# Kernel optimization log

Hardware: AMD Instinct MI355X
Metric: run time of the kernel (lower is better)

Reference implementation:

```python
import jax, jax.numpy as jnp
import numpy as np

K_V_DIM = 100
_SQRT_D = float(np.sqrt(K_V_DIM))


def _dk_layer(q, k, v, Wq, bq, Wk, n_unsqueeze):
    """One DKEncoder_layer: DK_text + DK_knowledge + DK_fusion (CokeBert attention).
    q: [B, q_dim]; k: [..., n, K_V_DIM]; v: [..., n, d_v].
    Attention over the last neighbor axis n.
    """
    # DK_text: linear + tanh + unsqueeze to broadcast against k
    q_i = jnp.tanh(q @ Wq.T + bq)                               # [B, D]
    q_i = q_i.reshape((q_i.shape[0],) + (1,) * n_unsqueeze + (K_V_DIM,))
    # DK_knowledge: bias-free linear on k
    k = k @ Wk.T
    # DK_fusion (CokeBert): scaled dot, mask zeros, leaky_relu+softmax, zero out fully-masked rows
    attn = (q_i * k).sum(-1) / _SQRT_D                          # [..., n]
    attn = jnp.where(attn == 0.0, -10000.0, attn)
    attn = jax.nn.softmax(jax.nn.leaky_relu(attn), axis=-1)
    n = attn.shape[-1]
    attn = jnp.where(attn == 1.0 / n, 0.0, attn)
    return jnp.einsum('...n,...nd->...d', attn, v)              # [..., d_v]


def setup_inputs() -> dict:
    key = jax.random.key(0)
    ks = jax.random.split(key, 12)
    B, S, E, N1, N2, D, Q = 8, 256, 256, 16, 16, K_V_DIM, 768
    return {
        "input_ent": jax.random.randint(ks[0], (B, S), 0, 2, dtype=jnp.int64),
        "q": jax.random.normal(ks[1], (B, S, Q), dtype=jnp.float32),
        "k1": jax.random.normal(ks[2], (B, E, N1, D), dtype=jnp.float32),
        "v1": jax.random.normal(ks[3], (B, E, N1, D), dtype=jnp.float32),
        "k2": jax.random.normal(ks[4], (B, E, N1, N2, D), dtype=jnp.float32),
        "v2": jax.random.normal(ks[5], (B, E, N1, N2, D), dtype=jnp.float32),
        # layers[0] has layer_no=2 (deepest), layers[1] has layer_no=1
        "Wq2": jax.random.normal(ks[6], (D, Q), dtype=jnp.float32) * 0.05,
        "bq2": jnp.zeros((D,), dtype=jnp.float32),
        "Wk2": jax.random.normal(ks[7], (D, D), dtype=jnp.float32) * 0.1,
        "Wq1": jax.random.normal(ks[8], (D, Q), dtype=jnp.float32) * 0.05,
        "bq1": jnp.zeros((D,), dtype=jnp.float32),
        "Wk1": jax.random.normal(ks[9], (D, D), dtype=jnp.float32) * 0.1,
    }


def reference(input_ent, q, k1, v1, k2, v2, Wq2, bq2, Wk2, Wq1, bq1, Wk1):
    q0 = q[:, 0, :]                                             # [B, Q]
    # layer 0 (layer_no=2): reduce innermost neighbor axis
    combined = _dk_layer(q0, k2, v2, Wq2, bq2, Wk2, 3)          # [B, E, N1, D]
    # layer 1 (layer_no=1): v = cat([v1, combined])
    v1c = jnp.concatenate([v1, combined], axis=-1)              # [B, E, N1, 2D]
    combined = _dk_layer(q0, k1, v1c, Wq1, bq1, Wk1, 2)         # [B, E, 2D]
    # scatter: i-th nonzero position of input_ent[b] receives combined[b, i]
    mask = input_ent != 0                                       # [B, S]
    rank = jnp.cumsum(mask.astype(jnp.int32), axis=1) - 1       # [B, S]
    rank = jnp.clip(rank, 0, combined.shape[1] - 1)
    gathered = jnp.take_along_axis(combined, rank[..., None], axis=1)  # [B, S, 2D]
    return jnp.where(mask[..., None], gathered, 0.0)
```

## Files before the change

### kernel.cpp

```cpp
#include <hip/hip_runtime.h>
#include <cstddef>
#include <cstdint>

#define BB 8
#define SS 256
#define EE 256
#define NN1 16
#define NN2 16
#define DD 100
#define QQ 768

__device__ __forceinline__ float dot4(float4 a, float4 b) {
    return a.x * b.x + a.y * b.y + a.z * b.z + a.w * b.w;
}

#define LGKM0() do { asm volatile("s_waitcnt lgkmcnt(0)" ::: "memory"); \
                     __builtin_amdgcn_sched_barrier(0); } while (0)

__global__ __launch_bounds__(256) void prep_kernel(
    const float* __restrict__ q, const int* __restrict__ ent,
    const float* __restrict__ Wq2, const float* __restrict__ bq2, const float* __restrict__ Wk2,
    const float* __restrict__ Wq1, const float* __restrict__ bq1, const float* __restrict__ Wk1,
    float* __restrict__ qk2o, float* __restrict__ qk1o, int* __restrict__ rk)
{
    const int blk = blockIdx.x, t = threadIdx.x;
    if (blk < 16) {
        const int b = blk >> 1, layer = blk & 1;
        const float* Wq = layer ? Wq1 : Wq2;
        const float* bq = layer ? bq1 : bq2;
        const float* Wk = layer ? Wk1 : Wk2;
        float* qko      = layer ? qk1o : qk2o;
        __shared__ float s_q[QQ];
        __shared__ float s_qi[DD];
        for (int i = t; i < QQ; i += 256) s_q[i] = q[(size_t)b * SS * QQ + i];
        __syncthreads();
        const float4* sq4 = (const float4*)s_q;
        const int r = t & 7;
        for (int d = t >> 3; d < DD; d += 32) {
            const float4* wq4 = (const float4*)(Wq + (size_t)d * QQ);
            float acc = 0.f;
            for (int c = r; c < QQ / 4; c += 8) acc += dot4(wq4[c], sq4[c]);
            acc += __shfl_xor(acc, 1, 8);
            acc += __shfl_xor(acc, 2, 8);
            acc += __shfl_xor(acc, 4, 8);
            if (r == 0) s_qi[d] = tanhf(acc + bq[d]);
        }
        __syncthreads();
        if (t < DD) {
            float acc = 0.f;
            for (int d = 0; d < DD; ++d) acc += s_qi[d] * Wk[d * DD + t];
            qko[b * DD + t] = 0.1f * acc;
        }
    } else {
        const int b = blk - 16;
        __shared__ int s_m[SS];
        const int m = (ent[b * SS + t] != 0) ? 1 : 0;
        s_m[t] = m;
        __syncthreads();
        for (int off = 1; off < SS; off <<= 1) {
            const int add = (t >= off) ? s_m[t - off] : 0;
            __syncthreads();
            s_m[t] += add;
            __syncthreads();
        }
        int rank = s_m[t] - 1;
        rank = rank < 0 ? 0 : (rank > EE - 1 ? EE - 1 : rank);
        rk[b * SS + t] = m ? rank : -1;
    }
}

__global__ __launch_bounds__(64) void dk2_kernel(
    const float* __restrict__ k2, const float* __restrict__ v2,
    const float* __restrict__ qk2g, float* __restrict__ c2o,
    int b0, int nunits)
{
    const int t = threadIdx.x;
    __shared__ float4 s_pp[400];
    float* s_part = (float*)s_pp;

    const int UPB = 8;
    int u = blockIdx.x * UPB;
    if (u >= nunits) return;
    const int uend = (u + UPB < nunits) ? u + UPB : nunits;
    const int b = b0 + (u >> 12);

    const float4* qkb = (const float4*)qk2g + (size_t)b * 25;
    float4 qv[7];
    #pragma unroll
    for (int j = 0; j < 6; ++j) qv[j] = qkb[(t + 64 * j) % 25];
    qv[6] = qkb[(384 + t) % 25];

    const float4* kt = (const float4*)k2 + ((size_t)b0 * 4096 + u) * 400;
    const float4* vt = (const float4*)v2 + ((size_t)b0 * 4096 + u) * 400;

    float4 ka[7];
    #pragma unroll
    for (int j = 0; j < 6; ++j) ka[j] = kt[t + 64 * j];
    if (t < 16) ka[6] = kt[384 + t];

    for (; u < uend; ++u, kt += 400, vt += 400) {
        float4 va[7];
        #pragma unroll
        for (int j = 0; j < 6; ++j) va[j] = vt[t + 64 * j];
        if (t < 16) va[6] = vt[384 + t];

        #pragma unroll
        for (int j = 0; j < 6; ++j) s_part[t + 64 * j] = dot4(ka[j], qv[j]);
        if (t < 16) s_part[384 + t] = dot4(ka[6], qv[6]);

        if (u + 1 < uend) {
            const float4* ktn = kt + 400;
            #pragma unroll
            for (int j = 0; j < 6; ++j) ka[j] = ktn[t + 64 * j];
            if (t < 16) ka[6] = ktn[384 + t];
        }

        LGKM0();
        float p;
        {
            float lg = 0.f;
            if (t < 16) {
                #pragma unroll
                for (int c = 0; c < 25; ++c) lg += s_part[t * 25 + c];
                if (lg == 0.0f) lg = -10000.0f;
                lg = lg >= 0.f ? lg : 0.01f * lg;
            }
            float mx = lg;
            mx = fmaxf(mx, __shfl_xor(mx, 1, 16));
            mx = fmaxf(mx, __shfl_xor(mx, 2, 16));
            mx = fmaxf(mx, __shfl_xor(mx, 4, 16));
            mx = fmaxf(mx, __shfl_xor(mx, 8, 16));
            const float e = __expf(lg - mx);
            float sm = e;
            sm += __shfl_xor(sm, 1, 16);
            sm += __shfl_xor(sm, 2, 16);
            sm += __shfl_xor(sm, 4, 16);
            sm += __shfl_xor(sm, 8, 16);
            p = e / sm;
            if (p == 0.0625f) p = 0.f;
        }

        #pragma unroll
        for (int j = 0; j < 6; ++j) {
            const int i = t + 64 * j;
            const float pn = __shfl(p, i / 25, 64);
            s_pp[i] = make_float4(pn * va[j].x, pn * va[j].y, pn * va[j].z, pn * va[j].w);
        }
        if (t < 16) {
            const int i = 384 + t;
            const float pn = __shfl(p, 15, 64);
            s_pp[i] = make_float4(pn * va[6].x, pn * va[6].y, pn * va[6].z, pn * va[6].w);
        }
        LGKM0();

        if (t < 25) {
            float4 a = make_float4(0.f, 0.f, 0.f, 0.f);
            #pragma unroll
            for (int n = 0; n < 16; ++n) {
                const float4 x = s_pp[n * 25 + t];
                a.x += x.x; a.y += x.y; a.z += x.z; a.w += x.w;
            }
            ((float4*)c2o)[(size_t)u * 25 + t] = a;
        }
    }
}

__global__ __launch_bounds__(64) void dk1_kernel(
    const float* __restrict__ k1, const float* __restrict__ v1,
    const float* __restrict__ c2i, const float* __restrict__ qk1g,
    float* __restrict__ comb, int b0)
{
    const int blk  = blockIdx.x;
    const int bbe  = blk >> 1;
    const int half = blk & 1;
    const int b    = b0 + (bbe >> 8);
    const int be   = (b << 8) | (bbe & 255);
    const int t    = threadIdx.x;

    __shared__ float4 s_pp[400];
    float* s_part = (float*)s_pp;

    const float4* kt = (const float4*)k1 + (size_t)be * 400;
    const float4* vt = half ? (const float4*)c2i + (size_t)bbe * 400
                            : (const float4*)v1 + (size_t)be * 400;
    const float4* qkb = (const float4*)qk1g + (size_t)b * 25;

    float4 qv[7];
    #pragma unroll
    for (int j = 0; j < 6; ++j) qv[j] = qkb[(t + 64 * j) % 25];
    qv[6] = qkb[(384 + t) % 25];

    float4 ka[7], va[7];
    #pragma unroll
    for (int j = 0; j < 6; ++j) { ka[j] = kt[t + 64 * j]; va[j] = vt[t + 64 * j]; }
    if (t < 16) { ka[6] = kt[384 + t]; va[6] = vt[384 + t]; }

    #pragma unroll
    for (int j = 0; j < 6; ++j) s_part[t + 64 * j] = dot4(ka[j], qv[j]);
    if (t < 16) s_part[384 + t] = dot4(ka[6], qv[6]);
    LGKM0();

    float p;
    {
        float lg = 0.f;
        if (t < 16) {
            #pragma unroll
            for (int c = 0; c < 25; ++c) lg += s_part[t * 25 + c];
            if (lg == 0.0f) lg = -10000.0f;
            lg = lg >= 0.f ? lg : 0.01f * lg;
        }
        float mx = lg;
        mx = fmaxf(mx, __shfl_xor(mx, 1, 16));
        mx = fmaxf(mx, __shfl_xor(mx, 2, 16));
        mx = fmaxf(mx, __shfl_xor(mx, 4, 16));
        mx = fmaxf(mx, __shfl_xor(mx, 8, 16));
        const float e = __expf(lg - mx);
        float sm = e;
        sm += __shfl_xor(sm, 1, 16);
        sm += __shfl_xor(sm, 2, 16);
        sm += __shfl_xor(sm, 4, 16);
        sm += __shfl_xor(sm, 8, 16);
        p = e / sm;
        if (p == 0.0625f) p = 0.f;
    }

    #pragma unroll
    for (int j = 0; j < 6; ++j) {
        const int i = t + 64 * j;
        const float pn = __shfl(p, i / 25, 64);
        s_pp[i] = make_float4(pn * va[j].x, pn * va[j].y, pn * va[j].z, pn * va[j].w);
    }
    if (t < 16) {
        const int i = 384 + t;
        const float pn = __shfl(p, 15, 64);
        s_pp[i] = make_float4(pn * va[6].x, pn * va[6].y, pn * va[6].z, pn * va[6].w);
    }
    LGKM0();

    if (t < 25) {
        float4 a = make_float4(0.f, 0.f, 0.f, 0.f);
        #pragma unroll
        for (int n = 0; n < 16; ++n) {
            const float4 x = s_pp[n * 25 + t];
            a.x += x.x; a.y += x.y; a.z += x.z; a.w += x.w;
        }
        ((float4*)comb)[(size_t)be * 50 + half * 25 + t] = a;
    }
}

__global__ __launch_bounds__(64) void gather_kernel(
    const float* __restrict__ comb, const int* __restrict__ rk, float* __restrict__ out)
{
    const int bs = blockIdx.x;
    const int b  = bs >> 8;
    const int t  = threadIdx.x;
    const int r  = rk[bs];
    float* o = out + (size_t)bs * (2 * DD);
    if (r < 0) {
        for (int d = t; d < 2 * DD; d += 64) o[d] = 0.f;
    } else {
        const float* src = comb + (size_t)(b * EE + r) * (2 * DD);
        for (int d = t; d < 2 * DD; d += 64) o[d] = src[d];
    }
}

extern "C" void kernel_launch(void* const* d_in, const int* in_sizes, int n_in,
                              void* d_out, int out_size, void* d_ws, size_t ws_size,
                              hipStream_t stream)
{
    const int*   ent = (const int*)d_in[0];
    const float* q   = (const float*)d_in[1];
    const float* k1  = (const float*)d_in[2];
    const float* v1  = (const float*)d_in[3];
    const float* k2  = (const float*)d_in[4];
    const float* v2  = (const float*)d_in[5];
    const float* Wq2 = (const float*)d_in[6];
    const float* bq2 = (const float*)d_in[7];
    const float* Wk2 = (const float*)d_in[8];
    const float* Wq1 = (const float*)d_in[9];
    const float* bq1 = (const float*)d_in[10];
    const float* Wk1 = (const float*)d_in[11];
    float* out = (float*)d_out;

    float* ws   = (float*)d_ws;
    float* qk2  = ws;
    float* qk1  = ws + 1024;
    int*   rk   = (int*)(ws + 2048);
    float* comb = ws + 4096;
    float* c2   = ws + 4096 + 409600;

    const size_t fixed = 4096 + 409600;
    const size_t perb  = (size_t)EE * NN1 * DD;
    size_t wsf = ws_size / sizeof(float);
    int kb = (wsf > fixed) ? (int)((wsf - fixed) / perb) : 1;
    if (kb < 1) kb = 1;
    if (kb > BB) kb = BB;

    prep_kernel<<<24, 256, 0, stream>>>(q, ent, Wq2, bq2, Wk2, Wq1, bq1, Wk1, qk2, qk1, rk);
    for (int b0 = 0; b0 < BB; b0 += kb) {
        const int nb = (BB - b0 < kb) ? (BB - b0) : kb;
        const int nunits = nb * EE * NN1;
        const int grid = (nunits + 7) / 8;
        dk2_kernel<<<grid, 64, 0, stream>>>(k2, v2, qk2, c2, b0, nunits);
        dk1_kernel<<<nb * EE * 2, 64, 0, stream>>>(k1, v1, c2, qk1, comb, b0);
    }
    gather_kernel<<<BB * SS, 64, 0, stream>>>(comb, rk, out);
}
```

Baseline: 157.1 us.

## Restructure dk2 kernel into a 256-thread block with a double-buffered load pipeline

The innermost attention kernel now runs 256 threads per block over 16 neighbor units each, instead of 64 threads over 8. It keeps K and V loads for two units in flight in registers. Dot-product partials and raw V go into double-buffered LDS. The probability-weighted V reduction is fused into the consume step through lane shuffles, instead of writing pre-scaled V to LDS. The aim is more memory-level parallelism and overlap of global loads with the softmax and reduction on this bandwidth-bound stage. The cost is explicit block barriers, softmax computed redundantly by all four waves, and only 25 lanes doing the final accumulation.

```diff
diff --git a/kernel.cpp b/kernel.cpp
--- a/kernel.cpp
+++ b/kernel.cpp
@@ -16,6 +16,9 @@
 
 #define LGKM0() do { asm volatile("s_waitcnt lgkmcnt(0)" ::: "memory"); \
                      __builtin_amdgcn_sched_barrier(0); } while (0)
+#define SCHED0() __builtin_amdgcn_sched_barrier(0)
+#define BARRIER() do { asm volatile("s_waitcnt lgkmcnt(0)\n\ts_barrier" ::: "memory"); \
+                       __builtin_amdgcn_sched_barrier(0); } while (0)
 
 __global__ __launch_bounds__(256) void prep_kernel(
     const float* __restrict__ q, const int* __restrict__ ent,
@@ -69,100 +72,115 @@
     }
 }
 
-__global__ __launch_bounds__(64) void dk2_kernel(
+__global__ __launch_bounds__(256, 4) void dk2_kernel(
     const float* __restrict__ k2, const float* __restrict__ v2,
     const float* __restrict__ qk2g, float* __restrict__ c2o,
     int b0, int nunits)
 {
     const int t = threadIdx.x;
-    __shared__ float4 s_pp[400];
-    float* s_part = (float*)s_pp;
-
-    const int UPB = 8;
-    int u = blockIdx.x * UPB;
-    if (u >= nunits) return;
-    const int uend = (u + UPB < nunits) ? u + UPB : nunits;
-    const int b = b0 + (u >> 12);
+    __shared__ float s_part[2][400];
+    __shared__ float s_v[2][1600];
+
+    const int base = blockIdx.x * 16;
+    if (base >= nunits) return;
+    const int b = b0 + (base >> 12);
 
     const float4* qkb = (const float4*)qk2g + (size_t)b * 25;
-    float4 qv[7];
-    #pragma unroll
-    for (int j = 0; j < 6; ++j) qv[j] = qkb[(t + 64 * j) % 25];
-    qv[6] = qkb[(384 + t) % 25];
-
-    const float4* kt = (const float4*)k2 + ((size_t)b0 * 4096 + u) * 400;
-    const float4* vt = (const float4*)v2 + ((size_t)b0 * 4096 + u) * 400;
-
-    float4 ka[7];
-    #pragma unroll
-    for (int j = 0; j < 6; ++j) ka[j] = kt[t + 64 * j];
-    if (t < 16) ka[6] = kt[384 + t];
-
-    for (; u < uend; ++u, kt += 400, vt += 400) {
-        float4 va[7];
-        #pragma unroll
-        for (int j = 0; j < 6; ++j) va[j] = vt[t + 64 * j];
-        if (t < 16) va[6] = vt[384 + t];
-
-        #pragma unroll
-        for (int j = 0; j < 6; ++j) s_part[t + 64 * j] = dot4(ka[j], qv[j]);
-        if (t < 16) s_part[384 + t] = dot4(ka[6], qv[6]);
-
-        if (u + 1 < uend) {
-            const float4* ktn = kt + 400;
-            #pragma unroll
-            for (int j = 0; j < 6; ++j) ka[j] = ktn[t + 64 * j];
-            if (t < 16) ka[6] = ktn[384 + t];
-        }
-
-        LGKM0();
-        float p;
-        {
-            float lg = 0.f;
-            if (t < 16) {
-                #pragma unroll
-                for (int c = 0; c < 25; ++c) lg += s_part[t * 25 + c];
-                if (lg == 0.0f) lg = -10000.0f;
-                lg = lg >= 0.f ? lg : 0.01f * lg;
-            }
-            float mx = lg;
-            mx = fmaxf(mx, __shfl_xor(mx, 1, 16));
-            mx = fmaxf(mx, __shfl_xor(mx, 2, 16));
-            mx = fmaxf(mx, __shfl_xor(mx, 4, 16));
-            mx = fmaxf(mx, __shfl_xor(mx, 8, 16));
-            const float e = __expf(lg - mx);
-            float sm = e;
-            sm += __shfl_xor(sm, 1, 16);
-            sm += __shfl_xor(sm, 2, 16);
-            sm += __shfl_xor(sm, 4, 16);
-            sm += __shfl_xor(sm, 8, 16);
-            p = e / sm;
-            if (p == 0.0625f) p = 0.f;
-        }
-
-        #pragma unroll
-        for (int j = 0; j < 6; ++j) {
-            const int i = t + 64 * j;
-            const float pn = __shfl(p, i / 25, 64);
-            s_pp[i] = make_float4(pn * va[j].x, pn * va[j].y, pn * va[j].z, pn * va[j].w);
-        }
-        if (t < 16) {
-            const int i = 384 + t;
-            const float pn = __shfl(p, 15, 64);
-            s_pp[i] = make_float4(pn * va[6].x, pn * va[6].y, pn * va[6].z, pn * va[6].w);
-        }
-        LGKM0();
-
-        if (t < 25) {
-            float4 a = make_float4(0.f, 0.f, 0.f, 0.f);
-            #pragma unroll
-            for (int n = 0; n < 16; ++n) {
-                const float4 x = s_pp[n * 25 + t];
-                a.x += x.x; a.y += x.y; a.z += x.z; a.w += x.w;
-            }
-            ((float4*)c2o)[(size_t)u * 25 + t] = a;
-        }
-    }
+    const float4 qv0 = qkb[t % 25];
+    const float4 qv1 = qkb[(t + 256) % 25];
+
+    const int  i0  = t;
+    const bool w1  = (t + 256 < 400);
+    const int  i1c = w1 ? t + 256 : 399;
+
+    const float4* kbase = (const float4*)k2 + ((size_t)b0 * 4096 + base) * 400;
+    const float4* vbase = (const float4*)v2 + ((size_t)b0 * 4096 + base) * 400;
+    float4* c2o4 = (float4*)c2o;
+
+    float4 kA0, kA1, vA0, vA1, kB0, kB1, vB0, vB1;
+
+#define ISSUE(K0, K1, V0, V1, ofs) do {                                     \
+        const float4* kp_ = kbase + (size_t)(ofs) * 400;                    \
+        const float4* vp_ = vbase + (size_t)(ofs) * 400;                    \
+        K0 = kp_[i0]; K1 = kp_[i1c]; V0 = vp_[i0]; V1 = vp_[i1c];           \
+    } while (0)
+
+#define DOTS(K0, K1, pb) do {                                               \
+        s_part[pb][i0] = dot4(K0, qv0);                                     \
+        if (w1) s_part[pb][t + 256] = dot4(K1, qv1);                        \
+    } while (0)
+
+#define VWRITE(V0, V1, sb) do {                                             \
+        ((float4*)s_v[sb])[i0] = V0;                                        \
+        if (w1) ((float4*)s_v[sb])[t + 256] = V1;                           \
+    } while (0)
+
+#define CONSUME(pb, sb, uu) do {                                            \
+        const int l_ = t & 15;                                              \
+        float lg_ = 0.f;                                                    \
+        _Pragma("unroll")                                                   \
+        for (int c_ = 0; c_ < 25; ++c_) lg_ += s_part[pb][l_ * 25 + c_];    \
+        if (lg_ == 0.0f) lg_ = -10000.0f;                                   \
+        lg_ = lg_ >= 0.f ? lg_ : 0.01f * lg_;               \
+        float mx_ = lg_;                                                    \
+        mx_ = fmaxf(mx_, __shfl_xor(mx_, 1, 16));                           \
+        mx_ = fmaxf(mx_, __shfl_xor(mx_, 2, 16));                           \
+        mx_ = fmaxf(mx_, __shfl_xor(mx_, 4, 16));                           \
+        mx_ = fmaxf(mx_, __shfl_xor(mx_, 8, 16));                           \
+        float e_ = __expf(lg_ - mx_);                                       \
+        float sm_ = e_;                                                     \
+        sm_ += __shfl_xor(sm_, 1, 16);                                      \
+        sm_ += __shfl_xor(sm_, 2, 16);                                      \
+        sm_ += __shfl_xor(sm_, 4, 16);                                      \
+        sm_ += __shfl_xor(sm_, 8, 16);                                      \
+        float p_ = e_ / sm_;                                                \
+        if (p_ == 0.0625f) p_ = 0.f;                    \
+        if (t < 25) {                                                       \
+            float ax = 0.f, ay = 0.f, az = 0.f, aw = 0.f;                   \
+            _Pragma("unroll")                                               \
+            for (int n_ = 0; n_ < 16; ++n_) {                               \
+                const float pn_ = __shfl(p_, n_, 64);   \
+                const float4 x_ = ((const float4*)s_v[sb])[n_ * 25 + t];    \
+                ax += pn_ * x_.x; ay += pn_ * x_.y;                         \
+                az += pn_ * x_.z; aw += pn_ * x_.w;                         \
+            }                                                               \
+            c2o4[(size_t)(uu) * 25 + t] = make_float4(ax, ay, az, aw);      \
+        }                                                                   \
+    } while (0)
+
+    ISSUE(kA0, kA1, vA0, vA1, 0);
+    ISSUE(kB0, kB1, vB0, vB1, 1);
+    SCHED0();
+    DOTS(kA0, kA1, 0);
+    VWRITE(vA0, vA1, 0);
+    BARRIER();
+
+    for (int g = 0; g < 7; ++g) {
+        const int x = 2 * g;
+        ISSUE(kA0, kA1, vA0, vA1, x + 2);
+        SCHED0();
+        CONSUME(0, 0, base + x);
+        DOTS(kB0, kB1, 1);
+        VWRITE(vB0, vB1, 1);
+        BARRIER();
+        ISSUE(kB0, kB1, vB0, vB1, x + 3);
+        SCHED0();
+        CONSUME(1, 1, base + x + 1);
+        DOTS(kA0, kA1, 0);
+        VWRITE(vA0, vA1, 0);
+        BARRIER();
+    }
+
+    CONSUME(0, 0, base + 14);
+    DOTS(kB0, kB1, 1);
+    VWRITE(vB0, vB1, 1);
+    BARRIER();
+    CONSUME(1, 1, base + 15);
+
+#undef ISSUE
+#undef DOTS
+#undef VWRITE
+#undef CONSUME
 }
 
 __global__ __launch_bounds__(64) void dk1_kernel(
@@ -300,8 +318,8 @@
     for (int b0 = 0; b0 < BB; b0 += kb) {
         const int nb = (BB - b0 < kb) ? (BB - b0) : kb;
         const int nunits = nb * EE * NN1;
-        const int grid = (nunits + 7) / 8;
-        dk2_kernel<<<grid, 64, 0, stream>>>(k2, v2, qk2, c2, b0, nunits);
+        const int grid = nunits / 16;
+        dk2_kernel<<<grid, 256, 0, stream>>>(k2, v2, qk2, c2, b0, nunits);
         dk1_kernel<<<nb * EE * 2, 64, 0, stream>>>(k1, v1, c2, qk1, comb, b0);
     }
     gather_kernel<<<BB * SS, 64, 0, stream>>>(comb, rk, out);
```

Result: slower. 163.3 us (+4.0%).

## Pipeline dk2 k/v loads into a 4-slot LDS ring via global_load_lds

Applied to the files above, without the earlier changes.

Rewrites the dominant dk2 kernel so each 64-thread block handles 64 units. K and V tiles stream directly from global memory into a 4-deep LDS ring buffer using async global_load_lds, and vmcnt waits keep up to three units in flight while the current one is computed. The dot products now run per row with 16-lane shuffle reductions, and the weighted V sum reads LDS directly. This is meant to hide HBM latency and cut register staging. In exchange it uses about 51KB of LDS per block, which limits occupancy, and it assumes nunits is divisible by 64 with hand-counted vmcnt values.

```diff
diff --git a/kernel.cpp b/kernel.cpp
--- a/kernel.cpp
+++ b/kernel.cpp
@@ -16,6 +16,7 @@
 
 #define LGKM0() do { asm volatile("s_waitcnt lgkmcnt(0)" ::: "memory"); \
                      __builtin_amdgcn_sched_barrier(0); } while (0)
+#define SCHED0() __builtin_amdgcn_sched_barrier(0)
 
 __global__ __launch_bounds__(256) void prep_kernel(
     const float* __restrict__ q, const int* __restrict__ ent,
@@ -75,94 +76,119 @@
     int b0, int nunits)
 {
     const int t = threadIdx.x;
-    __shared__ float4 s_pp[400];
-    float* s_part = (float*)s_pp;
-
-    const int UPB = 8;
-    int u = blockIdx.x * UPB;
-    if (u >= nunits) return;
-    const int uend = (u + UPB < nunits) ? u + UPB : nunits;
-    const int b = b0 + (u >> 12);
-
-    const float4* qkb = (const float4*)qk2g + (size_t)b * 25;
-    float4 qv[7];
-    #pragma unroll
-    for (int j = 0; j < 6; ++j) qv[j] = qkb[(t + 64 * j) % 25];
-    qv[6] = qkb[(384 + t) % 25];
-
-    const float4* kt = (const float4*)k2 + ((size_t)b0 * 4096 + u) * 400;
-    const float4* vt = (const float4*)v2 + ((size_t)b0 * 4096 + u) * 400;
-
-    float4 ka[7];
-    #pragma unroll
-    for (int j = 0; j < 6; ++j) ka[j] = kt[t + 64 * j];
-    if (t < 16) ka[6] = kt[384 + t];
-
-    for (; u < uend; ++u, kt += 400, vt += 400) {
-        float4 va[7];
-        #pragma unroll
-        for (int j = 0; j < 6; ++j) va[j] = vt[t + 64 * j];
-        if (t < 16) va[6] = vt[384 + t];
-
-        #pragma unroll
-        for (int j = 0; j < 6; ++j) s_part[t + 64 * j] = dot4(ka[j], qv[j]);
-        if (t < 16) s_part[384 + t] = dot4(ka[6], qv[6]);
-
-        if (u + 1 < uend) {
-            const float4* ktn = kt + 400;
-            #pragma unroll
-            for (int j = 0; j < 6; ++j) ka[j] = ktn[t + 64 * j];
-            if (t < 16) ka[6] = ktn[384 + t];
-        }
-
-        LGKM0();
-        float p;
-        {
-            float lg = 0.f;
-            if (t < 16) {
-                #pragma unroll
-                for (int c = 0; c < 25; ++c) lg += s_part[t * 25 + c];
-                if (lg == 0.0f) lg = -10000.0f;
-                lg = lg >= 0.f ? lg : 0.01f * lg;
-            }
-            float mx = lg;
-            mx = fmaxf(mx, __shfl_xor(mx, 1, 16));
-            mx = fmaxf(mx, __shfl_xor(mx, 2, 16));
-            mx = fmaxf(mx, __shfl_xor(mx, 4, 16));
-            mx = fmaxf(mx, __shfl_xor(mx, 8, 16));
-            const float e = __expf(lg - mx);
-            float sm = e;
-            sm += __shfl_xor(sm, 1, 16);
-            sm += __shfl_xor(sm, 2, 16);
-            sm += __shfl_xor(sm, 4, 16);
-            sm += __shfl_xor(sm, 8, 16);
-            p = e / sm;
-            if (p == 0.0625f) p = 0.f;
-        }
-
-        #pragma unroll
-        for (int j = 0; j < 6; ++j) {
-            const int i = t + 64 * j;
-            const float pn = __shfl(p, i / 25, 64);
-            s_pp[i] = make_float4(pn * va[j].x, pn * va[j].y, pn * va[j].z, pn * va[j].w);
-        }
-        if (t < 16) {
-            const int i = 384 + t;
-            const float pn = __shfl(p, 15, 64);
-            s_pp[i] = make_float4(pn * va[6].x, pn * va[6].y, pn * va[6].z, pn * va[6].w);
-        }
-        LGKM0();
-
-        if (t < 25) {
-            float4 a = make_float4(0.f, 0.f, 0.f, 0.f);
-            #pragma unroll
-            for (int n = 0; n < 16; ++n) {
-                const float4 x = s_pp[n * 25 + t];
-                a.x += x.x; a.y += x.y; a.z += x.z; a.w += x.w;
-            }
-            ((float4*)c2o)[(size_t)u * 25 + t] = a;
-        }
-    }
+    const int r = t & 15, g = t >> 4;
+    __shared__ float ring[4 * 3200];
+
+    const int UPB = 64;
+    const int u0 = blockIdx.x * UPB;
+    if (u0 >= nunits) return;
+    const int b = b0 + (u0 >> 12);
+
+    const float* qk = qk2g + (size_t)b * DD;
+    float qj[6];
+    #pragma unroll
+    for (int j = 0; j < 6; ++j) qj[j] = qk[r + 16 * j];
+    const float q6 = (r < 4) ? qk[96 + r] : 0.f;
+
+    const char* kgl = (const char*)(k2 + ((size_t)b0 * 4096 + u0) * 1600);
+    const char* vgl = (const char*)(v2 + ((size_t)b0 * 4096 + u0) * 1600);
+    auto g1k = (const __attribute__((address_space(1))) char*)kgl;
+    auto g1v = (const __attribute__((address_space(1))) char*)vgl;
+    auto l3  = (__attribute__((address_space(3))) char*)ring;
+
+#define ISSUE_UNIT(rel, slot) do {                                              \
+        const size_t gb_ = (size_t)(rel) * 6400;                                \
+        const int    lb_ = (slot) * 12800;                                      \
+        _Pragma("unroll")                                                       \
+        for (int j_ = 0; j_ < 6; ++j_) {                                        \
+            __builtin_amdgcn_global_load_lds(                                   \
+                (const __attribute__((address_space(1))) void*)(g1k + gb_ + j_ * 1024 + t * 16), \
+                (__attribute__((address_space(3))) void*)(l3 + lb_ + j_ * 1024), 16, 0, 0); \
+        }                                                                       \
+        __builtin_amdgcn_global_load_lds(                                       \
+            (const __attribute__((address_space(1))) void*)(g1k + gb_ + 5376 + t * 16), \
+            (__attribute__((address_space(3))) void*)(l3 + lb_ + 5376), 16, 0, 0); \
+        _Pragma("unroll")                                                       \
+        for (int j_ = 0; j_ < 6; ++j_) {                                        \
+            __builtin_amdgcn_global_load_lds(                                   \
+                (const __attribute__((address_space(1))) void*)(g1v + gb_ + j_ * 1024 + t * 16), \
+                (__attribute__((address_space(3))) void*)(l3 + lb_ + 6400 + j_ * 1024), 16, 0, 0); \
+        }                                                                       \
+        __builtin_amdgcn_global_load_lds(                                       \
+            (const __attribute__((address_space(1))) void*)(g1v + gb_ + 5376 + t * 16), \
+            (__attribute__((address_space(3))) void*)(l3 + lb_ + 6400 + 5376), 16, 0, 0); \
+    } while (0)
+
+#define COMPUTE_STORE(uu) do {                                                  \
+        const int   slot_ = (uu) & 3;                                           \
+        const float* Ks_ = ring + slot_ * 3200;                                 \
+        const float* Vs_ = Ks_ + 1600;                                          \
+        float lgv[4];                                                           \
+        _Pragma("unroll")                                                       \
+        for (int i_ = 0; i_ < 4; ++i_) {                                        \
+            const float* kr_ = Ks_ + (4 * g + i_) * DD;                         \
+            float s_ = kr_[r] * qj[0];                                          \
+            s_ += kr_[r + 16] * qj[1];                                          \
+            s_ += kr_[r + 32] * qj[2];                                          \
+            s_ += kr_[r + 48] * qj[3];                                          \
+            s_ += kr_[r + 64] * qj[4];                                          \
+            s_ += kr_[r + 80] * qj[5];                                          \
+            s_ += kr_[96 + r] * q6;       \
+            s_ += __shfl_xor(s_, 1, 16);                                        \
+            s_ += __shfl_xor(s_, 2, 16);                                        \
+            s_ += __shfl_xor(s_, 4, 16);                                        \
+            s_ += __shfl_xor(s_, 8, 16);                                        \
+            if (s_ == 0.0f) s_ = -10000.0f;                                     \
+            lgv[i_] = s_ >= 0.f ? s_ : 0.01f * s_;              \
+        }                                                                       \
+        float m_ = fmaxf(fmaxf(lgv[0], lgv[1]), fmaxf(lgv[2], lgv[3]));         \
+        m_ = fmaxf(m_, __shfl_xor(m_, 16, 64));                                 \
+        m_ = fmaxf(m_, __shfl_xor(m_, 32, 64));                                 \
+        const float e0_ = __expf(lgv[0] - m_), e1_ = __expf(lgv[1] - m_);       \
+        const float e2_ = __expf(lgv[2] - m_), e3_ = __expf(lgv[3] - m_);       \
+        float sm_ = e0_ + e1_ + e2_ + e3_;                                      \
+        sm_ += __shfl_xor(sm_, 16, 64);                                         \
+        sm_ += __shfl_xor(sm_, 32, 64);                                         \
+        float p0_ = e0_ / sm_; if (p0_ == 0.0625f) p0_ = 0.f;                   \
+        float p1_ = e1_ / sm_; if (p1_ == 0.0625f) p1_ = 0.f;                   \
+        float p2_ = e2_ / sm_; if (p2_ == 0.0625f) p2_ = 0.f;                   \
+        float p3_ = e3_ / sm_; if (p3_ == 0.0625f) p3_ = 0.f;                   \
+        float a0_ = 0.f, a1_ = 0.f;                                             \
+        _Pragma("unroll")                                                       \
+        for (int n_ = 0; n_ < 16; ++n_) {                                       \
+            float ps_;                                                          \
+            switch (n_ & 3) {                                                   \
+                case 0: ps_ = p0_; break;                                       \
+                case 1: ps_ = p1_; break;                                       \
+                case 2: ps_ = p2_; break;                                       \
+                default: ps_ = p3_; break;                                      \
+            }                                                                   \
+            const float pn_ = __shfl(ps_, (n_ >> 2) * 16, 64);                  \
+            a0_ += pn_ * Vs_[n_ * DD + t];                                      \
+            a1_ += pn_ * Vs_[n_ * DD + 64 + t];  \
+        }                                                                       \
+        float* o_ = c2o + (size_t)(u0 + (uu)) * DD;                             \
+        o_[t] = a0_;                                                            \
+        if (t < 36) o_[64 + t] = a1_;                                           \
+    } while (0)
+
+    ISSUE_UNIT(0, 0); ISSUE_UNIT(1, 1); ISSUE_UNIT(2, 2); ISSUE_UNIT(3, 3);
+
+    int u = 0;
+    for (; u < UPB - 4; ++u) {
+        asm volatile("s_waitcnt vmcnt(42)" ::: "memory");
+        SCHED0();
+        COMPUTE_STORE(u);
+        SCHED0();
+        ISSUE_UNIT(u + 4, u & 3);
+    }
+    asm volatile("s_waitcnt vmcnt(42)" ::: "memory"); SCHED0(); COMPUTE_STORE(UPB - 4);
+    asm volatile("s_waitcnt vmcnt(28)" ::: "memory"); SCHED0(); COMPUTE_STORE(UPB - 3);
+    asm volatile("s_waitcnt vmcnt(14)" ::: "memory"); SCHED0(); COMPUTE_STORE(UPB - 2);
+    asm volatile("s_waitcnt vmcnt(0)"  ::: "memory"); SCHED0(); COMPUTE_STORE(UPB - 1);
+
+#undef ISSUE_UNIT
+#undef COMPUTE_STORE
 }
 
 __global__ __launch_bounds__(64) void dk1_kernel(
@@ -300,7 +326,7 @@
     for (int b0 = 0; b0 < BB; b0 += kb) {
         const int nb = (BB - b0 < kb) ? (BB - b0) : kb;
         const int nunits = nb * EE * NN1;
-        const int grid = (nunits + 7) / 8;
+        const int grid = nunits / 64;
         dk2_kernel<<<grid, 64, 0, stream>>>(k2, v2, qk2, c2, b0, nunits);
         dk1_kernel<<<nb * EE * 2, 64, 0, stream>>>(k1, v1, c2, qk1, comb, b0);
     }
```

Result: slower. 168.5 us (+7.3%).
